# Kernel tuning notes

Measured on AMD Instinct MI355X. Metric: run time of the kernel, lower is better.

Reference implementation:

```python
import jax, jax.numpy as jnp
import numpy as np

D_MODEL = 1024
H = 16
D_K = D_MODEL // H
D_FF = 4096
EPS = 1e-6


def layer_norm(x, alpha, bias):
    mean = jnp.mean(x, axis=-1, keepdims=True)
    var = jnp.mean((x - mean) ** 2, axis=-1, keepdims=True)  # unbiased=False
    return alpha * (x - mean) / jnp.sqrt(var + EPS) + bias


def setup_inputs() -> dict:
    key = jax.random.key(0)
    ks = jax.random.split(key, 8)
    B, S = 4, 2048
    sd = 1.0 / np.sqrt(D_MODEL)
    x = jax.random.normal(ks[0], (B, S, D_MODEL), dtype=jnp.float32)
    src_mask = jnp.ones((B, 1, S), dtype=jnp.int32)
    wq = jax.random.normal(ks[1], (D_MODEL, D_MODEL), jnp.float32) * sd
    wk = jax.random.normal(ks[2], (D_MODEL, D_MODEL), jnp.float32) * sd
    wv = jax.random.normal(ks[3], (D_MODEL, D_MODEL), jnp.float32) * sd
    wo = jax.random.normal(ks[4], (D_MODEL, D_MODEL), jnp.float32) * sd
    w1 = jax.random.normal(ks[5], (D_FF, D_MODEL), jnp.float32) * sd
    b1 = jnp.zeros((D_FF,), jnp.float32)
    w2 = jax.random.normal(ks[6], (D_MODEL, D_FF), jnp.float32) * (1.0 / np.sqrt(D_FF))
    b2 = jnp.zeros((D_MODEL,), jnp.float32)
    ln1_a = jnp.ones((D_MODEL,), jnp.float32)
    ln1_b = jnp.zeros((D_MODEL,), jnp.float32)
    ln2_a = jnp.ones((D_MODEL,), jnp.float32)
    ln2_b = jnp.zeros((D_MODEL,), jnp.float32)
    return dict(x=x, src_mask=src_mask, wq=wq, wk=wk, wv=wv, wo=wo,
                ln1_a=ln1_a, ln1_b=ln1_b, ln2_a=ln2_a, ln2_b=ln2_b,
                w1=w1, b1=b1, w2=w2, b2=b2)


def attention(xn, wq, wk, wv, wo, src_mask):
    B, S, _ = xn.shape
    # torch nn.Linear: y = x @ W.T
    q = (xn @ wq.T).reshape(B, S, H, D_K).transpose(0, 2, 1, 3)  # [B,H,S,Dk]
    k = (xn @ wk.T).reshape(B, S, H, D_K).transpose(0, 2, 1, 3)
    v = (xn @ wv.T).reshape(B, S, H, D_K).transpose(0, 2, 1, 3)
    scores = jnp.einsum('bhqd,bhkd->bhqk', q, k) / np.sqrt(D_K)
    m = src_mask[:, None, :, :]  # [B,1,1,S] from [B,1,S]
    scores = jnp.where(m == 0, -jnp.inf, scores)
    attn = jax.nn.softmax(scores, axis=-1)
    out = jnp.einsum('bhqk,bhkd->bhqd', attn, v)
    out = out.transpose(0, 2, 1, 3).reshape(B, S, D_MODEL)
    return out @ wo.T


def reference(x, src_mask, wq, wk, wv, wo, ln1_a, ln1_b, ln2_a, ln2_b, w1, b1, w2, b2):
    # pre-LN residual 1: self-attention
    xn = layer_norm(x, ln1_a, ln1_b)
    x = x + attention(xn, wq, wk, wv, wo, src_mask)
    # pre-LN residual 2: FFN
    xn = layer_norm(x, ln2_a, ln2_b)
    h = jax.nn.relu(xn @ w1.T + b1)
    x = x + (h @ w2.T + b2)
    return x
```

## Files before the change

### kernel.cpp

```cpp
#include <hip/hip_runtime.h>
#include <stdint.h>

typedef unsigned short u16;
typedef __bf16 bf16x8 __attribute__((ext_vector_type(8)));
typedef float   f32x4 __attribute__((ext_vector_type(4)));
typedef u16     u16x8 __attribute__((ext_vector_type(8)));
typedef u16     u16x4 __attribute__((ext_vector_type(4)));

__device__ __forceinline__ float bf2f(u16 u) {
    union { uint32_t i; float f; } c; c.i = ((uint32_t)u) << 16; return c.f;
}
__device__ __forceinline__ u16 f2bf(float f) {
    union { float f; uint32_t i; } c; c.f = f;
    uint32_t r = c.i + 0x7FFFu + ((c.i >> 16) & 1u);
    return (u16)(r >> 16);
}
__device__ __forceinline__ u16 f2bf_fast(float f) {
    union { float f; uint32_t i; } c; c.f = f;
    return (u16)((c.i + 0x8000u) >> 16);
}
__device__ __forceinline__ uint32_t cvt_pk_bf16(float lo, float hi) {
    uint32_t r;
    asm("v_cvt_pk_bf16_f32 %0, %1, %2" : "=v"(r) : "v"(lo), "v"(hi));
    return r;
}
__device__ __forceinline__ void gload_lds16(const u16* g, u16* l) {
    __builtin_amdgcn_global_load_lds(
        (__attribute__((address_space(1))) void*)(g),
        (__attribute__((address_space(3))) void*)(l), 16, 0, 0);
}

__global__ __launch_bounds__(256) void cvt_all(
    const float* __restrict__ wq, const float* __restrict__ wk,
    const float* __restrict__ wv, const float* __restrict__ wo,
    const float* __restrict__ w1, const float* __restrict__ w2,
    u16* __restrict__ wqb, u16* __restrict__ wkb, u16* __restrict__ wvb,
    u16* __restrict__ wob, u16* __restrict__ w1b, u16* __restrict__ w2b)
{
    int blk = blockIdx.x;
    const float* src; u16* dst; int off;
    if      (blk < 1024)  { src = wq; dst = wqb; off = blk; }
    else if (blk < 2048)  { src = wk; dst = wkb; off = blk - 1024; }
    else if (blk < 3072)  { src = wv; dst = wvb; off = blk - 2048; }
    else if (blk < 4096)  { src = wo; dst = wob; off = blk - 3072; }
    else if (blk < 8192)  { src = w1; dst = w1b; off = blk - 4096; }
    else                  { src = w2; dst = w2b; off = blk - 8192; }
    int i = off * 1024 + threadIdx.x * 4;
    float4 v = *(const float4*)(src + i);
    u16x4 o; o[0] = f2bf(v.x); o[1] = f2bf(v.y); o[2] = f2bf(v.z); o[3] = f2bf(v.w);
    *(u16x4*)(dst + i) = o;
}

__global__ __launch_bounds__(256) void ln_kernel(
    const float* __restrict__ x, const float* __restrict__ ga,
    const float* __restrict__ be, u16* __restrict__ out)
{
    const int D = 1024;
    int row  = blockIdx.x * 4 + (threadIdx.x >> 6);
    int lane = threadIdx.x & 63;
    const float* xr = x + (size_t)row * D + lane * 16;
    float f[16];
#pragma unroll
    for (int i = 0; i < 4; ++i) *(float4*)&f[i * 4] = *(const float4*)(xr + i * 4);
    float s = 0.f, s2 = 0.f;
#pragma unroll
    for (int i = 0; i < 16; ++i) { s += f[i]; s2 += f[i] * f[i]; }
#pragma unroll
    for (int off = 1; off < 64; off <<= 1) {
        s  += __shfl_xor(s,  off, 64);
        s2 += __shfl_xor(s2, off, 64);
    }
    float mean = s * (1.0f / 1024.0f);
    float var  = s2 * (1.0f / 1024.0f) - mean * mean;
    var = var < 0.f ? 0.f : var;
    float inv = 1.0f / sqrtf(var + 1e-6f);
    float g[16], b[16];
#pragma unroll
    for (int i = 0; i < 4; ++i) {
        *(float4*)&g[i * 4] = *(const float4*)(ga + lane * 16 + i * 4);
        *(float4*)&b[i * 4] = *(const float4*)(be + lane * 16 + i * 4);
    }
    u16x8 o0, o1;
#pragma unroll
    for (int i = 0; i < 8; ++i) {
        o0[i] = f2bf(g[i]     * (f[i]     - mean) * inv + b[i]);
        o1[i] = f2bf(g[8 + i] * (f[8 + i] - mean) * inv + b[8 + i]);
    }
    u16* orow = out + (size_t)row * D + lane * 16;
    *(u16x8*)(orow)     = o0;
    *(u16x8*)(orow + 8) = o1;
}

__device__ __forceinline__ void gemm_core(
    const u16* __restrict__ A, const u16* __restrict__ W,
    int K, int ldw, int row_a0, int row_w0,
    u16* As, u16* Bs, f32x4 (&acc)[4][4])
{
    int tid  = threadIdx.x;
    int lane = tid & 63;
    int quad = (lane >> 4), l16 = lane & 15;
    int wave = tid >> 6;
    int wr = wave >> 1, wc = wave & 1;
    int srow = tid >> 2, scol = (tid & 3) * 8;
    const u16* a0p = A + (size_t)(row_a0 + srow) * K + scol;
    const u16* a1p = a0p + (size_t)64 * K;
    const u16* b0p = W + (size_t)(row_w0 + srow) * ldw + scol;
    const u16* b1p = b0p + (size_t)64 * ldw;
    u16* la0 = As + tid * 8;
    u16* la1 = As + 2048 + tid * 8;
    u16* la2 = As + 4096 + tid * 8;
    u16* la3 = As + 6144 + tid * 8;
    u16* lb0 = Bs + tid * 8;
    u16* lb1 = Bs + 2048 + tid * 8;
    u16* lb2 = Bs + 4096 + tid * 8;
    u16* lb3 = Bs + 6144 + tid * 8;

    for (int k0 = 0; k0 < K; k0 += 64) {
        __syncthreads();
        gload_lds16(a0p + k0,      la0);
        gload_lds16(a1p + k0,      la1);
        gload_lds16(a0p + k0 + 32, la2);
        gload_lds16(a1p + k0 + 32, la3);
        gload_lds16(b0p + k0,      lb0);
        gload_lds16(b1p + k0,      lb1);
        gload_lds16(b0p + k0 + 32, lb2);
        gload_lds16(b1p + k0 + 32, lb3);
        __syncthreads();
#pragma unroll
        for (int h = 0; h < 2; ++h) {
            const u16* Ah = As + h * 4096;
            const u16* Bh = Bs + h * 4096;
            bf16x8 af[4], bf[4];
#pragma unroll
            for (int mt = 0; mt < 4; ++mt)
                af[mt] = *(const bf16x8*)(&Ah[(wr * 64 + mt * 16 + l16) * 32 + quad * 8]);
#pragma unroll
            for (int nt = 0; nt < 4; ++nt)
                bf[nt] = *(const bf16x8*)(&Bh[(wc * 64 + nt * 16 + l16) * 32 + quad * 8]);
#pragma unroll
            for (int mt = 0; mt < 4; ++mt)
#pragma unroll
                for (int nt = 0; nt < 4; ++nt)
                    acc[mt][nt] = __builtin_amdgcn_mfma_f32_16x16x32_bf16(
                        af[mt], bf[nt], acc[mt][nt], 0, 0, 0);
        }
    }
}

template<bool OUTF32>
__global__ __launch_bounds__(256) void gemm128(
    const u16* __restrict__ A, const u16* __restrict__ W,
    const float* __restrict__ bias, const float* __restrict__ resid,
    void* __restrict__ Cp, int M, int N, int K, int ldw, int do_relu)
{
    __shared__ u16 As[128 * 64];
    __shared__ u16 Bs[128 * 64];
    int tid  = threadIdx.x;
    int lane = tid & 63, wave = tid >> 6;
    int quad = lane >> 4, l16 = lane & 15;
    int wr = wave >> 1, wc = wave & 1;
    const int row_a0 = blockIdx.x * 128, row_w0 = blockIdx.y * 128;
    f32x4 acc[4][4] = {};
    gemm_core(A, W, K, ldw, row_a0, row_w0, As, Bs, acc);
#pragma unroll
    for (int mt = 0; mt < 4; ++mt) {
#pragma unroll
        for (int nt = 0; nt < 4; ++nt) {
#pragma unroll
            for (int r = 0; r < 4; ++r) {
                int grow = row_a0 + wr * 64 + mt * 16 + quad * 4 + r;
                int gcol = row_w0 + wc * 64 + nt * 16 + l16;
                float vv = acc[mt][nt][r];
                if (bias)    vv += bias[gcol];
                if (do_relu) vv = vv > 0.f ? vv : 0.f;
                if (resid)   vv += resid[(size_t)grow * N + gcol];
                if (OUTF32) ((float*)Cp)[(size_t)grow * N + gcol] = vv;
                else        ((u16*)Cp)[(size_t)grow * N + gcol] = f2bf(vv);
            }
        }
    }
}

__global__ __launch_bounds__(256) void gemm128_qkv(
    const u16* __restrict__ A, const u16* __restrict__ Wqkv,
    u16* __restrict__ qo, u16* __restrict__ ko, u16* __restrict__ vo, int K)
{
    __shared__ u16 As[128 * 64];
    __shared__ u16 Bs[128 * 64];
    int tid  = threadIdx.x;
    int lane = tid & 63, wave = tid >> 6;
    int quad = lane >> 4, l16 = lane & 15;
    int wr = wave >> 1, wc = wave & 1;
    const int row_a0 = blockIdx.x * 128, row_w0 = blockIdx.y * 128;
    f32x4 acc[4][4] = {};
    gemm_core(A, Wqkv, K, K, row_a0, row_w0, As, Bs, acc);
    int seg = row_w0 >> 10;
    u16* dst = (seg == 0) ? qo : (seg == 1) ? ko : vo;
    int col0 = row_w0 & 1023;
#pragma unroll
    for (int mt = 0; mt < 4; ++mt) {
#pragma unroll
        for (int nt = 0; nt < 4; ++nt) {
#pragma unroll
            for (int r = 0; r < 4; ++r) {
                int grow = row_a0 + wr * 64 + mt * 16 + quad * 4 + r;
                int gcol = col0 + wc * 64 + nt * 16 + l16;
                dst[(size_t)grow * 1024 + gcol] = f2bf(acc[mt][nt][r]);
            }
        }
    }
}

__global__ __launch_bounds__(512, 4) void attn_kernel(
    const u16* __restrict__ Q, const u16* __restrict__ Km, const u16* __restrict__ Vm,
    const int* __restrict__ mask, u16* __restrict__ O)
{
    const int S = 2048, DM = 1024;
    const float C1 = 0.18033688f;
    const float C0 = -11.541560f;
    __shared__ u16 Qs[128][72];
    __shared__ u16 Ks[64 * 64];
    __shared__ u16 Vt[64][72];
    __shared__ u16 Ps[128][72];

    int qt = blockIdx.x, bh = blockIdx.y;
    int b = bh >> 4, h = bh & 15;
    int tid = threadIdx.x;
    int wave = tid >> 6, lane = tid & 63;
    int quad = lane >> 4, l16 = lane & 15;
    size_t base = (size_t)b * S;
    size_t hoff = (size_t)h * 64;

    {
        int r = tid >> 2, c0 = (tid & 3) * 16;
        const u16* src = Q + (base + qt * 128 + r) * DM + hoff + c0;
        *(u16x8*)(&Qs[r][c0])     = *(const u16x8*)(src);
        *(u16x8*)(&Qs[r][c0 + 8]) = *(const u16x8*)(src + 8);
    }
    const u16* ksrc = Km + (base + (tid >> 3)) * DM + hoff
                    + ((tid & 7) ^ ((tid >> 5) & 7)) * 8;
    u16* kdst = Ks + tid * 8;
    int kp = tid & 31, d0 = (tid >> 5) * 4;
    const u16* vsrc = Vm + (base + kp * 2) * DM + hoff + d0;
    const int* msrc = mask + b * S + 4 * l16;

    __syncthreads();
    const int q0 = wave * 16;
    bf16x8 qf0 = *(const bf16x8*)(&Qs[q0 + l16][quad * 8]);
    bf16x8 qf1 = *(const bf16x8*)(&Qs[q0 + l16][32 + quad * 8]);
    const int swz = (l16 & 7) * 8;
    const int u0  = (quad * 8) ^ swz;

    float l_r[4] = {0.f, 0.f, 0.f, 0.f};
    f32x4 o[4] = {};

    for (int it = 0; it < 32; ++it) {
        __syncthreads();
        gload_lds16(ksrc, kdst);
        ksrc += 64 * DM;
        {
            u16x4 va = *(const u16x4*)(vsrc);
            u16x4 vb = *(const u16x4*)(vsrc + DM);
            vsrc += 64 * DM;
#pragma unroll
            for (int i = 0; i < 4; ++i) {
                uint32_t w = (uint32_t)va[i] | ((uint32_t)vb[i] << 16);
                *(uint32_t*)(&Vt[d0 + i][kp * 2]) = w;
            }
        }
        __syncthreads();
        f32x4 sc[4] = {};
#pragma unroll
        for (int t = 0; t < 4; ++t) {
            const u16* krp = Ks + (4 * l16 + t) * 64;
            bf16x8 kf0 = *(const bf16x8*)(krp + u0);
            bf16x8 kf1 = *(const bf16x8*)(krp + (u0 ^ 32));
            sc[t] = __builtin_amdgcn_mfma_f32_16x16x32_bf16(qf0, kf0, sc[t], 0, 0, 0);
            sc[t] = __builtin_amdgcn_mfma_f32_16x16x32_bf16(qf1, kf1, sc[t], 0, 0, 0);
        }
        int4 mk4 = *(const int4*)(msrc); msrc += 64;
        float c0t[4];
        c0t[0] = (mk4.x == 0) ? -1e38f : C0;
        c0t[1] = (mk4.y == 0) ? -1e38f : C0;
        c0t[2] = (mk4.z == 0) ? -1e38f : C0;
        c0t[3] = (mk4.w == 0) ? -1e38f : C0;
#pragma unroll
        for (int r = 0; r < 4; ++r) {
            float p0 = exp2f(fmaf(sc[0][r], C1, c0t[0]));
            float p1 = exp2f(fmaf(sc[1][r], C1, c0t[1]));
            float p2 = exp2f(fmaf(sc[2][r], C1, c0t[2]));
            float p3 = exp2f(fmaf(sc[3][r], C1, c0t[3]));
            l_r[r] += (p0 + p1) + (p2 + p3);
            int prow = q0 + quad * 4 + r;
            uint2 pw;
            pw.x = cvt_pk_bf16(p0, p1);
            pw.y = cvt_pk_bf16(p2, p3);
            *(uint2*)(&Ps[prow][4 * l16]) = pw;
        }
        bf16x8 pf0 = *(const bf16x8*)(&Ps[q0 + l16][quad * 8]);
        bf16x8 pf1 = *(const bf16x8*)(&Ps[q0 + l16][32 + quad * 8]);
#pragma unroll
        for (int t = 0; t < 4; ++t) {
            bf16x8 vf0 = *(const bf16x8*)(&Vt[t * 16 + l16][quad * 8]);
            bf16x8 vf1 = *(const bf16x8*)(&Vt[t * 16 + l16][32 + quad * 8]);
            o[t] = __builtin_amdgcn_mfma_f32_16x16x32_bf16(pf0, vf0, o[t], 0, 0, 0);
            o[t] = __builtin_amdgcn_mfma_f32_16x16x32_bf16(pf1, vf1, o[t], 0, 0, 0);
        }
    }
#pragma unroll
    for (int r = 0; r < 4; ++r) {
#pragma unroll
        for (int off = 1; off < 16; off <<= 1) l_r[r] += __shfl_xor(l_r[r], off, 16);
        float inv = 1.0f / l_r[r];
        u16* dst = O + (base + qt * 128 + q0 + quad * 4 + r) * DM + hoff + l16;
#pragma unroll
        for (int t = 0; t < 4; ++t) dst[t * 16] = f2bf(o[t][r] * inv);
    }
}

extern "C" void kernel_launch(void* const* d_in, const int* in_sizes, int n_in,
                              void* d_out, int out_size, void* d_ws, size_t ws_size,
                              hipStream_t stream)
{
    (void)in_sizes; (void)n_in; (void)out_size; (void)ws_size;
    const float* x    = (const float*)d_in[0];
    const int*   mask = (const int*)d_in[1];
    const float* wq   = (const float*)d_in[2];
    const float* wk   = (const float*)d_in[3];
    const float* wv   = (const float*)d_in[4];
    const float* wo   = (const float*)d_in[5];
    const float* ln1a = (const float*)d_in[6];
    const float* ln1b = (const float*)d_in[7];
    const float* ln2a = (const float*)d_in[8];
    const float* ln2b = (const float*)d_in[9];
    const float* w1   = (const float*)d_in[10];
    const float* b1   = (const float*)d_in[11];
    const float* w2   = (const float*)d_in[12];
    const float* b2   = (const float*)d_in[13];

    const int M = 8192, D = 1024, F = 4096;
    char* ws = (char*)d_ws;
    u16*  wqkv = (u16*)(ws);
    u16*  wqb = wqkv;
    u16*  wkb = (u16*)(ws + (2u  << 20));
    u16*  wvb = (u16*)(ws + (4u  << 20));
    u16*  wob = (u16*)(ws + (6u  << 20));
    u16*  w1b = (u16*)(ws + (8u  << 20));
    u16*  w2b = (u16*)(ws + (16u << 20));
    u16*  xn  = (u16*)(ws + (24u << 20));
    u16*  q   = (u16*)(ws + (40u << 20));
    u16*  hb  = (u16*)(ws + (40u << 20));

    u16*   kbuf = (u16*)d_out;
    u16*   vbuf = (u16*)d_out + (size_t)M * D;
    float* x1   = (float*)d_out;

    cvt_all<<<12288, 256, 0, stream>>>(wq, wk, wv, wo, w1, w2,
                                       wqb, wkb, wvb, wob, w1b, w2b);

    ln_kernel<<<M / 4, 256, 0, stream>>>(x, ln1a, ln1b, xn);
    dim3 gq(M / 128, 3072 / 128);
    gemm128_qkv<<<gq, 256, 0, stream>>>(xn, wqkv, q, kbuf, vbuf, D);
    dim3 ga(2048 / 128, 64);
    attn_kernel<<<ga, 512, 0, stream>>>(q, kbuf, vbuf, mask, xn);
    dim3 g1(M / 128, D / 128);
    gemm128<true ><<<g1, 256, 0, stream>>>(xn, wob, nullptr, x, x1, M, D, D, D, 0);
    ln_kernel<<<M / 4, 256, 0, stream>>>(x1, ln2a, ln2b, xn);
    dim3 gf1(M / 128, 2048 / 128);
    dim3 gf2(M / 128, D / 128);
    gemm128<false><<<gf1, 256, 0, stream>>>(xn, w1b, b1, nullptr, hb, M, 2048, D, D, 1);
    gemm128<true ><<<gf2, 256, 0, stream>>>(hb, w2b, nullptr, x1, x1, M, D, 2048, F, 0);
    gemm128<false><<<gf1, 256, 0, stream>>>(xn, w1b + (size_t)2048 * D, b1 + 2048, nullptr, hb, M, 2048, D, D, 1);
    gemm128<true ><<<gf2, 256, 0, stream>>>(hb, w2b + 2048, b2, x1, x1, M, D, 2048, F, 0);
}
```

Before: 667.2 us.

## Double-buffer K/V tiles in attention kernel with one barrier per iteration

The attention kernel now ping-pongs between two K and V^T LDS buffers. The next tile's K async load and V global loads are issued before the current tile's QK^T and PV MFMAs, and the transposed V is written to LDS afterwards. This drops one of the two block-wide barriers per iteration and overlaps global-memory latency with compute. The Q staging buffer is aliased onto the second buffer to keep total LDS the same, at the cost of V values held in registers across the compute phase.

```diff
diff --git a/kernel.cpp b/kernel.cpp
--- a/kernel.cpp
+++ b/kernel.cpp
@@ -218,10 +218,13 @@
     const int S = 2048, DM = 1024;
     const float C1 = 0.18033688f;
     const float C0 = -11.541560f;
-    __shared__ u16 Qs[128][72];
-    __shared__ u16 Ks[64 * 64];
-    __shared__ u16 Vt[64][72];
-    __shared__ u16 Ps[128][72];
+    __shared__ u16 smem[27136];
+    u16* Qs  = smem;
+    u16* Ks1 = smem;
+    u16* Vt1 = smem + 4096;
+    u16* Ks0 = smem + 9216;
+    u16* Vt0 = smem + 13312;
+    u16* Ps  = smem + 17920;
 
     int qt = blockIdx.x, bh = blockIdx.y;
     int b = bh >> 4, h = bh & 15;
@@ -234,45 +237,55 @@
     {
         int r = tid >> 2, c0 = (tid & 3) * 16;
         const u16* src = Q + (base + qt * 128 + r) * DM + hoff + c0;
-        *(u16x8*)(&Qs[r][c0])     = *(const u16x8*)(src);
-        *(u16x8*)(&Qs[r][c0 + 8]) = *(const u16x8*)(src + 8);
+        *(u16x8*)(&Qs[r * 72 + c0])     = *(const u16x8*)(src);
+        *(u16x8*)(&Qs[r * 72 + c0 + 8]) = *(const u16x8*)(src + 8);
     }
     const u16* ksrc = Km + (base + (tid >> 3)) * DM + hoff
                     + ((tid & 7) ^ ((tid >> 5) & 7)) * 8;
-    u16* kdst = Ks + tid * 8;
     int kp = tid & 31, d0 = (tid >> 5) * 4;
     const u16* vsrc = Vm + (base + kp * 2) * DM + hoff + d0;
     const int* msrc = mask + b * S + 4 * l16;
 
     __syncthreads();
     const int q0 = wave * 16;
-    bf16x8 qf0 = *(const bf16x8*)(&Qs[q0 + l16][quad * 8]);
-    bf16x8 qf1 = *(const bf16x8*)(&Qs[q0 + l16][32 + quad * 8]);
+    bf16x8 qf0 = *(const bf16x8*)(&Qs[(q0 + l16) * 72 + quad * 8]);
+    bf16x8 qf1 = *(const bf16x8*)(&Qs[(q0 + l16) * 72 + 32 + quad * 8]);
     const int swz = (l16 & 7) * 8;
     const int u0  = (quad * 8) ^ swz;
 
+    {
+        u16x4 va = *(const u16x4*)(vsrc);
+        u16x4 vb = *(const u16x4*)(vsrc + DM);
+        gload_lds16(ksrc, Ks0 + tid * 8);
+        ksrc += 64 * DM; vsrc += 64 * DM;
+#pragma unroll
+        for (int i = 0; i < 4; ++i) {
+            uint32_t w = (uint32_t)va[i] | ((uint32_t)vb[i] << 16);
+            *(uint32_t*)(&Vt0[(d0 + i) * 72 + kp * 2]) = w;
+        }
+    }
+    __syncthreads();
+
     float l_r[4] = {0.f, 0.f, 0.f, 0.f};
     f32x4 o[4] = {};
 
     for (int it = 0; it < 32; ++it) {
-        __syncthreads();
-        gload_lds16(ksrc, kdst);
-        ksrc += 64 * DM;
-        {
-            u16x4 va = *(const u16x4*)(vsrc);
-            u16x4 vb = *(const u16x4*)(vsrc + DM);
-            vsrc += 64 * DM;
-#pragma unroll
-            for (int i = 0; i < 4; ++i) {
-                uint32_t w = (uint32_t)va[i] | ((uint32_t)vb[i] << 16);
-                *(uint32_t*)(&Vt[d0 + i][kp * 2]) = w;
-            }
-        }
-        __syncthreads();
+        const u16* Kcur = (it & 1) ? Ks1 : Ks0;
+        const u16* Vcur = (it & 1) ? Vt1 : Vt0;
+        u16* Knxt = (it & 1) ? Ks0 : Ks1;
+        u16* Vnxt = (it & 1) ? Vt0 : Vt1;
+        const bool pfch = (it < 31);
+        u16x4 va, vb;
+        if (pfch) {
+            va = *(const u16x4*)(vsrc);
+            vb = *(const u16x4*)(vsrc + DM);
+            gload_lds16(ksrc, Knxt + tid * 8);
+            ksrc += 64 * DM; vsrc += 64 * DM;
+        }
         f32x4 sc[4] = {};
 #pragma unroll
         for (int t = 0; t < 4; ++t) {
-            const u16* krp = Ks + (4 * l16 + t) * 64;
+            const u16* krp = Kcur + (4 * l16 + t) * 64;
             bf16x8 kf0 = *(const bf16x8*)(krp + u0);
             bf16x8 kf1 = *(const bf16x8*)(krp + (u0 ^ 32));
             sc[t] = __builtin_amdgcn_mfma_f32_16x16x32_bf16(qf0, kf0, sc[t], 0, 0, 0);
@@ -295,17 +308,25 @@
             uint2 pw;
             pw.x = cvt_pk_bf16(p0, p1);
             pw.y = cvt_pk_bf16(p2, p3);
-            *(uint2*)(&Ps[prow][4 * l16]) = pw;
-        }
-        bf16x8 pf0 = *(const bf16x8*)(&Ps[q0 + l16][quad * 8]);
-        bf16x8 pf1 = *(const bf16x8*)(&Ps[q0 + l16][32 + quad * 8]);
+            *(uint2*)(&Ps[prow * 72 + 4 * l16]) = pw;
+        }
+        bf16x8 pf0 = *(const bf16x8*)(&Ps[(q0 + l16) * 72 + quad * 8]);
+        bf16x8 pf1 = *(const bf16x8*)(&Ps[(q0 + l16) * 72 + 32 + quad * 8]);
 #pragma unroll
         for (int t = 0; t < 4; ++t) {
-            bf16x8 vf0 = *(const bf16x8*)(&Vt[t * 16 + l16][quad * 8]);
-            bf16x8 vf1 = *(const bf16x8*)(&Vt[t * 16 + l16][32 + quad * 8]);
+            bf16x8 vf0 = *(const bf16x8*)(&Vcur[(t * 16 + l16) * 72 + quad * 8]);
+            bf16x8 vf1 = *(const bf16x8*)(&Vcur[(t * 16 + l16) * 72 + 32 + quad * 8]);
             o[t] = __builtin_amdgcn_mfma_f32_16x16x32_bf16(pf0, vf0, o[t], 0, 0, 0);
             o[t] = __builtin_amdgcn_mfma_f32_16x16x32_bf16(pf1, vf1, o[t], 0, 0, 0);
         }
+        if (pfch) {
+#pragma unroll
+            for (int i = 0; i < 4; ++i) {
+                uint32_t w = (uint32_t)va[i] | ((uint32_t)vb[i] << 16);
+                *(uint32_t*)(&Vnxt[(d0 + i) * 72 + kp * 2]) = w;
+            }
+        }
+        __syncthreads();
     }
 #pragma unroll
     for (int r = 0; r < 4; ++r) {
```

After: 637.8 us. -4.4%, faster.
